# Performance work log

Measured on AMD Instinct MI355X. Metric: run time of the kernel, lower is better.

## Reference

```python
import jax, jax.numpy as jnp
import numpy as np
import math

N_HEADS = 16
D_HEAD = 64
DEPTH = 12
LAMBDA_INIT = 0.8 - 0.6 * math.exp(-0.3 * DEPTH)
SCALING = 1.0 / math.sqrt(D_HEAD)
RMS_EPS = 1e-6
B, T = 4, 1024


def setup_inputs() -> dict:
    key = jax.random.key(0)
    ks = jax.random.split(key, 8)
    q = jax.random.normal(ks[0], (B, 2 * N_HEADS, T, D_HEAD), dtype=jnp.float32)
    k = jax.random.normal(ks[1], (B, 2 * N_HEADS, T, D_HEAD), dtype=jnp.float32)
    v = jax.random.normal(ks[2], (B, N_HEADS, T, 2 * D_HEAD), dtype=jnp.float32)
    # causal mask, broadcast over batch/heads; masked_fill where mask == 0
    mask = jnp.tril(jnp.ones((1, 1, T, T), dtype=jnp.int32))
    lambda_q1 = 0.1 * jax.random.normal(ks[3], (N_HEADS, D_HEAD), dtype=jnp.float32)
    lambda_k1 = 0.1 * jax.random.normal(ks[4], (N_HEADS, D_HEAD), dtype=jnp.float32)
    lambda_q2 = 0.1 * jax.random.normal(ks[5], (N_HEADS, D_HEAD), dtype=jnp.float32)
    lambda_k2 = 0.1 * jax.random.normal(ks[6], (N_HEADS, D_HEAD), dtype=jnp.float32)
    rms_weight = jnp.ones((2 * D_HEAD,), dtype=jnp.float32)
    return {"q": q, "k": k, "v": v, "mask": mask,
            "lambda_q1": lambda_q1, "lambda_k1": lambda_k1,
            "lambda_q2": lambda_q2, "lambda_k2": lambda_k2,
            "rms_weight": rms_weight, "flash_attn": 0}


def _rms_norm(x, weight):
    var = jnp.mean(jnp.square(x), axis=-1, keepdims=True)
    return x * jax.lax.rsqrt(var + RMS_EPS) * weight


def reference(q, k, v, mask, lambda_q1, lambda_k1, lambda_q2, lambda_k2, rms_weight, flash_attn):
    # lambda reparameterization: scalar per head
    lambda_1 = jnp.exp(jnp.sum(lambda_q1 * lambda_k1, axis=-1))  # [H]
    lambda_2 = jnp.exp(jnp.sum(lambda_q2 * lambda_k2, axis=-1))  # [H]
    lambda_final = lambda_1 - lambda_2 + LAMBDA_INIT             # [H]

    Bq, H2, Tq, Dh = q.shape
    # dual attention scores over 2*n_heads heads: [B, 2H, T, T]
    attn = jnp.einsum('bhtd,bhsd->bhts', q, k) * SCALING
    attn = jnp.where(mask == 0, -jnp.inf, attn)
    attn = jax.nn.softmax(attn.astype(jnp.float32), axis=-1).astype(q.dtype)
    # consecutive head pairs -> (attn1, attn2)
    attn = attn.reshape(Bq, H2 // 2, 2, Tq, Tq)
    attn = attn[:, :, 0] - lambda_final[None, :, None, None] * attn[:, :, 1]
    # dropout is identity in eval mode
    y = jnp.einsum('bhts,bhsd->bhtd', attn, v)  # [B, H, T, 2*d_head]
    y = _rms_norm(y, rms_weight)
    y = y * (1.0 - LAMBDA_INIT)
    return y
```

## Files before the change

kernel.cpp:

```cpp
#include <hip/hip_runtime.h>


typedef _Float16 f16x4 __attribute__((ext_vector_type(4)));
typedef _Float16 f16x8 __attribute__((ext_vector_type(8)));
typedef float    f32x4 __attribute__((ext_vector_type(4)));

constexpr int   TSEQ        = 1024;
constexpr int   DQK         = 64;
constexpr int   DVDIM       = 128;
constexpr float SCALING     = 0.125f;
constexpr float LAMBDA_INIT = 0.7836057665316245f;
constexpr float ONE_MINUS_LI= 1.0f - LAMBDA_INIT;
constexpr float RMS_EPS     = 1e-6f;
constexpr float LOG2E       = 1.4426950408889634f;

__global__ __launch_bounds__(256, 2)
void diff_attn_kernel(const float* __restrict__ qg, const float* __restrict__ kg,
                      const float* __restrict__ vg,
                      const float* __restrict__ lq1, const float* __restrict__ lk1,
                      const float* __restrict__ lq2, const float* __restrict__ lk2,
                      const float* __restrict__ rmsw, float* __restrict__ out)
{
    __shared__ _Float16 Klds[2][64][72];
    __shared__ _Float16 Vt[128][68];

    const int a    = blockIdx.x;
    const int hp   = blockIdx.y;
    const int b    = blockIdx.z;
    const int t    = threadIdx.x;
    const int w    = t >> 6;
    const int lane = t & 63;
    const int n    = lane & 15;
    const int quad = lane >> 4;

    float a1 = lq1[hp*64 + lane] * lk1[hp*64 + lane];
    float a2 = lq2[hp*64 + lane] * lk2[hp*64 + lane];
    #pragma unroll
    for (int d = 1; d < 64; d <<= 1) { a1 += __shfl_xor(a1, d); a2 += __shfl_xor(a2, d); }
    const float lambda = __expf(a1) - __expf(a2) + LAMBDA_INIT;

    const float* kb = kg + ((size_t)(b*32 + hp*2)) * TSEQ * DQK;
    const float* vb = vg + ((size_t)(b*16 + hp))   * TSEQ * DVDIM;

    const int jj   = t & 15;
    const int sg   = t >> 4;
    const int dvb  = jj * 8;
    const int s0   = sg * 4;
    const int rotw = (jj & 7) * 8;
    const int d8   = t & 7;

    float4 kr[4][2], vr[8];

    auto load_tile = [&](int sbase) {
        #pragma unroll
        for (int i = 0; i < 4; ++i) {
            const int row = (i*256 + t) >> 3;
            const int h = row >> 6, sr = row & 63;
            const float* p = kb + ((size_t)h*TSEQ + sbase + sr)*DQK + d8*8;
            kr[i][0] = *(const float4*)p;
            kr[i][1] = *(const float4*)(p + 4);
        }
        const float* vp = vb + (size_t)(sbase + s0)*DVDIM + dvb;
        #pragma unroll
        for (int r = 0; r < 4; ++r) {
            vr[2*r]   = *(const float4*)(vp + r*DVDIM);
            vr[2*r+1] = *(const float4*)(vp + r*DVDIM + 4);
        }
    };

    auto write_tile = [&]() {
        #pragma unroll
        for (int i = 0; i < 4; ++i) {
            const int row = (i*256 + t) >> 3;
            const int h = row >> 6, sr = row & 63;
            f16x8 kk;
            kk[0]=(_Float16)kr[i][0].x; kk[1]=(_Float16)kr[i][0].y;
            kk[2]=(_Float16)kr[i][0].z; kk[3]=(_Float16)kr[i][0].w;
            kk[4]=(_Float16)kr[i][1].x; kk[5]=(_Float16)kr[i][1].y;
            kk[6]=(_Float16)kr[i][1].z; kk[7]=(_Float16)kr[i][1].w;
            *(f16x8*)&Klds[h][sr][d8*8] = kk;
        }
        float vrow[4][8];
        #pragma unroll
        for (int r = 0; r < 4; ++r) {
            vrow[r][0]=vr[2*r].x;   vrow[r][1]=vr[2*r].y;
            vrow[r][2]=vr[2*r].z;   vrow[r][3]=vr[2*r].w;
            vrow[r][4]=vr[2*r+1].x; vrow[r][5]=vr[2*r+1].y;
            vrow[r][6]=vr[2*r+1].z; vrow[r][7]=vr[2*r+1].w;
        }
        #pragma unroll
        for (int mI = 0; mI < 8; ++mI) {
            f16x4 pk;
            pk[0]=(_Float16)vrow[0][mI]; pk[1]=(_Float16)vrow[1][mI];
            pk[2]=(_Float16)vrow[2][mI]; pk[3]=(_Float16)vrow[3][mI];
            *(f16x4*)&Vt[dvb + mI][(s0 + rotw) & 63] = pk;
        }
    };

    const float qscale = SCALING * LOG2E;
    load_tile(0);

    for (int part = 0; part < 2; ++part) {
        const int qt    = part ? (15 - a) : a;
        const int qbase = qt * 64;
        const int qw0   = qbase + w * 16;
        const int qrow  = qw0 + n;
        const int nT    = qt + 1;

        f16x8 Qf[2][2];
        #pragma unroll
        for (int h = 0; h < 2; ++h) {
            const float* qp = qg + (((size_t)(b*32 + hp*2 + h)) * TSEQ + qrow) * DQK + quad*8;
            #pragma unroll
            for (int ks = 0; ks < 2; ++ks) {
                float4 x = *(const float4*)(qp + ks*32);
                float4 y = *(const float4*)(qp + ks*32 + 4);
                f16x8 f;
                f[0]=(_Float16)(x.x*qscale); f[1]=(_Float16)(x.y*qscale);
                f[2]=(_Float16)(x.z*qscale); f[3]=(_Float16)(x.w*qscale);
                f[4]=(_Float16)(y.x*qscale); f[5]=(_Float16)(y.y*qscale);
                f[6]=(_Float16)(y.z*qscale); f[7]=(_Float16)(y.w*qscale);
                Qf[h][ks] = f;
            }
        }

        f32x4 O[2][8];
        #pragma unroll
        for (int h = 0; h < 2; ++h)
            #pragma unroll
            for (int d = 0; d < 8; ++d) O[h][d] = (f32x4){0.f,0.f,0.f,0.f};
        float m_[2] = { -__builtin_huge_valf(), -__builtin_huge_valf() };
        float l_[2] = { 0.f, 0.f };

        for (int tile = 0; tile < nT; ++tile) {
            const int sbase = tile * 64;
            __syncthreads();
            write_tile();
            __syncthreads();
            if (tile + 1 < nT)      load_tile((tile + 1) * 64);
            else if (part == 0)     load_tile(0);

            const bool diag = (tile == qt);
            const int  nact = diag ? (w + 1) : 4;

            f16x4 pb[2][4];
            #pragma unroll
            for (int h = 0; h < 2; ++h) {
                f32x4 St[4];
                #pragma unroll
                for (int sub = 0; sub < 4; ++sub) {
                    if (sub < nact) {
                        f16x8 k0 = *(const f16x8*)&Klds[h][sub*16 + n][quad*8];
                        f16x8 k1 = *(const f16x8*)&Klds[h][sub*16 + n][32 + quad*8];
                        f32x4 c = (f32x4){0.f,0.f,0.f,0.f};
                        c = __builtin_amdgcn_mfma_f32_16x16x32_f16(k0, Qf[h][0], c, 0, 0, 0);
                        c = __builtin_amdgcn_mfma_f32_16x16x32_f16(k1, Qf[h][1], c, 0, 0, 0);
                        St[sub] = c;
                    }
                }
                float vals[16];
                #pragma unroll
                for (int sub = 0; sub < 4; ++sub) {
                    if (sub < nact) {
                        #pragma unroll
                        for (int r = 0; r < 4; ++r) {
                            const int s = sbase + sub*16 + quad*4 + r;
                            float x = St[sub][r];
                            if (diag && s > qrow) x = -__builtin_huge_valf();
                            vals[sub*4 + r] = x;
                        }
                    }
                }
                float mx = -__builtin_huge_valf();
                #pragma unroll
                for (int sub = 0; sub < 4; ++sub)
                    if (sub < nact)
                        #pragma unroll
                        for (int r = 0; r < 4; ++r) mx = fmaxf(mx, vals[sub*4 + r]);
                mx = fmaxf(mx, __shfl_xor(mx, 16));
                mx = fmaxf(mx, __shfl_xor(mx, 32));
                const float mold  = m_[h];
                const float mnew  = fmaxf(mold, mx);
                const float alpha = exp2f(mold - mnew);
                float rs = 0.f;
                #pragma unroll
                for (int sub = 0; sub < 4; ++sub) {
                    if (sub < nact) {
                        #pragma unroll
                        for (int r = 0; r < 4; ++r) {
                            const float p = exp2f(vals[sub*4 + r] - mnew);
                            rs += p;
                            pb[h][sub][r] = (_Float16)p;
                        }
                    }
                }
                rs += __shfl_xor(rs, 16);
                rs += __shfl_xor(rs, 32);
                m_[h] = mnew;
                l_[h] = l_[h] * alpha + rs;
                #pragma unroll
                for (int d = 0; d < 8; ++d) {
                    O[h][d][0] *= alpha; O[h][d][1] *= alpha;
                    O[h][d][2] *= alpha; O[h][d][3] *= alpha;
                }
            }
            #pragma unroll
            for (int dd = 0; dd < 8; ++dd) {
                const int rot_r = ((2*dd + (n >> 3)) & 7) * 8;
                #pragma unroll
                for (int sub = 0; sub < 4; ++sub) {
                    if (sub < nact) {
                        f16x4 va = *(const f16x4*)&Vt[dd*16 + n][(sub*16 + quad*4 + rot_r) & 63];
                        O[0][dd] = __builtin_amdgcn_mfma_f32_16x16x16f16(va, pb[0][sub], O[0][dd], 0, 0, 0);
                        O[1][dd] = __builtin_amdgcn_mfma_f32_16x16x16f16(va, pb[1][sub], O[1][dd], 0, 0, 0);
                    }
                }
            }
        }

        const float i1 = 1.0f   / l_[0];
        const float i2 = lambda / l_[1];
        float yv[8][4];
        float ss = 0.f;
        #pragma unroll
        for (int d = 0; d < 8; ++d)
            #pragma unroll
            for (int r = 0; r < 4; ++r) {
                const float y = O[0][d][r] * i1 - O[1][d][r] * i2;
                yv[d][r] = y; ss += y * y;
            }
        ss += __shfl_xor(ss, 16);
        ss += __shfl_xor(ss, 32);
        const float sc = rsqrtf(ss * (1.0f/128.0f) + RMS_EPS) * ONE_MINUS_LI;

        float* ob = out + (((size_t)(b*16 + hp)) * TSEQ + qrow) * DVDIM;
        #pragma unroll
        for (int d = 0; d < 8; ++d) {
            const int dv = d*16 + quad*4;
            float4 wv = *(const float4*)&rmsw[dv];
            float4 o;
            o.x = yv[d][0] * sc * wv.x;
            o.y = yv[d][1] * sc * wv.y;
            o.z = yv[d][2] * sc * wv.z;
            o.w = yv[d][3] * sc * wv.w;
            *(float4*)(ob + dv) = o;
        }
    }
}

extern "C" void kernel_launch(void* const* d_in, const int* in_sizes, int n_in,
                              void* d_out, int out_size, void* d_ws, size_t ws_size,
                              hipStream_t stream) {
    const float* q    = (const float*)d_in[0];
    const float* k    = (const float*)d_in[1];
    const float* v    = (const float*)d_in[2];
    const float* lq1  = (const float*)d_in[4];
    const float* lk1  = (const float*)d_in[5];
    const float* lq2  = (const float*)d_in[6];
    const float* lk2  = (const float*)d_in[7];
    const float* rmsw = (const float*)d_in[8];
    float* out = (float*)d_out;

    dim3 grid(8, 16, 4);
    dim3 block(256);
    diff_attn_kernel<<<grid, block, 0, stream>>>(q, k, v, lq1, lk1, lq2, lk2, rmsw, out);
}
```

Baseline: 224.5 us.

## Convert prefetched K/V to fp16 at load, skip redundant rescale, remap grid

Prefetched K and V tiles are converted to fp16 immediately after the global loads, which halves the registers held across the compute loop. The output-accumulator rescale is skipped when no row maximum changed anywhere in the wavefront. The 3D grid becomes a 1D grid whose block index is decoded so that neighbouring blocks share different head/batch groups, which spreads work across XCDs and caches. The lambda computation is moved after the first tile prefetch so it overlaps load latency. The trade-off is that the conversion work now sits right after each load, and the skip adds a wave vote plus a branch.

```diff
diff --git a/kernel.cpp b/kernel.cpp
--- a/kernel.cpp
+++ b/kernel.cpp
@@ -24,20 +24,18 @@
     __shared__ _Float16 Klds[2][64][72];
     __shared__ _Float16 Vt[128][68];
 
-    const int a    = blockIdx.x;
-    const int hp   = blockIdx.y;
-    const int b    = blockIdx.z;
+    const int lin = blockIdx.x;
+    const int xs  = lin & 7;
+    const int a   = (lin >> 3) & 7;
+    const int g   = xs + ((lin >> 6) << 3);
+    const int hp  = g & 15;
+    const int b   = g >> 4;
+
     const int t    = threadIdx.x;
     const int w    = t >> 6;
     const int lane = t & 63;
     const int n    = lane & 15;
     const int quad = lane >> 4;
-
-    float a1 = lq1[hp*64 + lane] * lk1[hp*64 + lane];
-    float a2 = lq2[hp*64 + lane] * lk2[hp*64 + lane];
-    #pragma unroll
-    for (int d = 1; d < 64; d <<= 1) { a1 += __shfl_xor(a1, d); a2 += __shfl_xor(a2, d); }
-    const float lambda = __expf(a1) - __expf(a2) + LAMBDA_INIT;
 
     const float* kb = kg + ((size_t)(b*32 + hp*2)) * TSEQ * DQK;
     const float* vb = vg + ((size_t)(b*16 + hp))   * TSEQ * DVDIM;
@@ -49,7 +47,8 @@
     const int rotw = (jj & 7) * 8;
     const int d8   = t & 7;
 
-    float4 kr[4][2], vr[8];
+    f16x8 kr16[4];
+    f16x4 vr16[4][2];
 
     auto load_tile = [&](int sbase) {
         #pragma unroll
@@ -57,14 +56,20 @@
             const int row = (i*256 + t) >> 3;
             const int h = row >> 6, sr = row & 63;
             const float* p = kb + ((size_t)h*TSEQ + sbase + sr)*DQK + d8*8;
-            kr[i][0] = *(const float4*)p;
-            kr[i][1] = *(const float4*)(p + 4);
+            float4 x = *(const float4*)p;
+            float4 y = *(const float4*)(p + 4);
+            f16x8 kk;
+            kk[0]=(_Float16)x.x; kk[1]=(_Float16)x.y; kk[2]=(_Float16)x.z; kk[3]=(_Float16)x.w;
+            kk[4]=(_Float16)y.x; kk[5]=(_Float16)y.y; kk[6]=(_Float16)y.z; kk[7]=(_Float16)y.w;
+            kr16[i] = kk;
         }
         const float* vp = vb + (size_t)(sbase + s0)*DVDIM + dvb;
         #pragma unroll
         for (int r = 0; r < 4; ++r) {
-            vr[2*r]   = *(const float4*)(vp + r*DVDIM);
-            vr[2*r+1] = *(const float4*)(vp + r*DVDIM + 4);
+            float4 x = *(const float4*)(vp + r*DVDIM);
+            float4 y = *(const float4*)(vp + r*DVDIM + 4);
+            vr16[r][0] = (f16x4){(_Float16)x.x,(_Float16)x.y,(_Float16)x.z,(_Float16)x.w};
+            vr16[r][1] = (f16x4){(_Float16)y.x,(_Float16)y.y,(_Float16)y.z,(_Float16)y.w};
         }
     };
 
@@ -73,32 +78,29 @@
         for (int i = 0; i < 4; ++i) {
             const int row = (i*256 + t) >> 3;
             const int h = row >> 6, sr = row & 63;
-            f16x8 kk;
-            kk[0]=(_Float16)kr[i][0].x; kk[1]=(_Float16)kr[i][0].y;
-            kk[2]=(_Float16)kr[i][0].z; kk[3]=(_Float16)kr[i][0].w;
-            kk[4]=(_Float16)kr[i][1].x; kk[5]=(_Float16)kr[i][1].y;
-            kk[6]=(_Float16)kr[i][1].z; kk[7]=(_Float16)kr[i][1].w;
-            *(f16x8*)&Klds[h][sr][d8*8] = kk;
-        }
-        float vrow[4][8];
-        #pragma unroll
-        for (int r = 0; r < 4; ++r) {
-            vrow[r][0]=vr[2*r].x;   vrow[r][1]=vr[2*r].y;
-            vrow[r][2]=vr[2*r].z;   vrow[r][3]=vr[2*r].w;
-            vrow[r][4]=vr[2*r+1].x; vrow[r][5]=vr[2*r+1].y;
-            vrow[r][6]=vr[2*r+1].z; vrow[r][7]=vr[2*r+1].w;
+            *(f16x8*)&Klds[h][sr][d8*8] = kr16[i];
         }
         #pragma unroll
         for (int mI = 0; mI < 8; ++mI) {
+            const int hh = mI >> 2, ee = mI & 3;
             f16x4 pk;
-            pk[0]=(_Float16)vrow[0][mI]; pk[1]=(_Float16)vrow[1][mI];
-            pk[2]=(_Float16)vrow[2][mI]; pk[3]=(_Float16)vrow[3][mI];
+            pk[0] = vr16[0][hh][ee];
+            pk[1] = vr16[1][hh][ee];
+            pk[2] = vr16[2][hh][ee];
+            pk[3] = vr16[3][hh][ee];
             *(f16x4*)&Vt[dvb + mI][(s0 + rotw) & 63] = pk;
         }
     };
 
+    load_tile(0);
+
+    float a1 = lq1[hp*64 + lane] * lk1[hp*64 + lane];
+    float a2 = lq2[hp*64 + lane] * lk2[hp*64 + lane];
+    #pragma unroll
+    for (int d = 1; d < 64; d <<= 1) { a1 += __shfl_xor(a1, d); a2 += __shfl_xor(a2, d); }
+    const float lambda = __expf(a1) - __expf(a2) + LAMBDA_INIT;
+
     const float qscale = SCALING * LOG2E;
-    load_tile(0);
 
     for (int part = 0; part < 2; ++part) {
         const int qt    = part ? (15 - a) : a;
@@ -137,8 +139,8 @@
             __syncthreads();
             write_tile();
             __syncthreads();
-            if (tile + 1 < nT)      load_tile((tile + 1) * 64);
-            else if (part == 0)     load_tile(0);
+            if (tile + 1 < nT)  load_tile((tile + 1) * 64);
+            else if (part == 0) load_tile(0);
 
             const bool diag = (tile == qt);
             const int  nact = diag ? (w + 1) : 4;
@@ -198,10 +200,12 @@
                 rs += __shfl_xor(rs, 32);
                 m_[h] = mnew;
                 l_[h] = l_[h] * alpha + rs;
-                #pragma unroll
-                for (int d = 0; d < 8; ++d) {
-                    O[h][d][0] *= alpha; O[h][d][1] *= alpha;
-                    O[h][d][2] *= alpha; O[h][d][3] *= alpha;
+                if (!__all(mnew == mold)) {
+                    #pragma unroll
+                    for (int d = 0; d < 8; ++d) {
+                        O[h][d][0] *= alpha; O[h][d][1] *= alpha;
+                        O[h][d][2] *= alpha; O[h][d][3] *= alpha;
+                    }
                 }
             }
             #pragma unroll
@@ -261,7 +265,7 @@
     const float* rmsw = (const float*)d_in[8];
     float* out = (float*)d_out;
 
-    dim3 grid(8, 16, 4);
+    dim3 grid(512, 1, 1);
     dim3 block(256);
     diff_attn_kernel<<<grid, block, 0, stream>>>(q, k, v, lq1, lk1, lq2, lk2, rmsw, out);
 }
```

New measurement: 261.1 us. 16.3% more time.
